# Kernel optimization log

Measured on AMD Instinct MI355X. Metric: run time of the kernel, lower is better.

## Reference

```python
import jax, jax.numpy as jnp
import numpy as np

B, IN_DIM, T = 4, 512, 4096
EMBED, HEADS, NB_FEAT = 1024, 16, 256
D_HEAD = EMBED // HEADS
EPS = 1e-6


def _orthogonal_random_matrix(key, nb_rows, nb_cols):
    # scaling==1 branch: sqrt(nb_cols) * Q from reduced QR of a Gaussian block
    block = jax.random.normal(key, (nb_rows, nb_cols), dtype=jnp.float32)
    q, _ = jnp.linalg.qr(block)
    return jnp.sqrt(jnp.float32(nb_cols)) * q


def setup_inputs() -> dict:
    key = jax.random.key(0)
    kx, kq, kk, kv, ko, kp = jax.random.split(key, 6)
    s = 1.0 / np.sqrt(IN_DIM)
    return {
        "x": jax.random.normal(kx, (B, IN_DIM, T), dtype=jnp.float32),
        "Wq": jax.random.normal(kq, (IN_DIM, EMBED), dtype=jnp.float32) * s,
        "Wk": jax.random.normal(kk, (IN_DIM, EMBED), dtype=jnp.float32) * s,
        "Wv": jax.random.normal(kv, (IN_DIM, EMBED), dtype=jnp.float32) * s,
        "Wo": jax.random.normal(ko, (EMBED, EMBED), dtype=jnp.float32) * (1.0 / np.sqrt(EMBED)),
        "proj": _orthogonal_random_matrix(kp, NB_FEAT, D_HEAD),
    }


def reference(x, Wq, Wk, Wv, Wo, proj):
    b, c, t = x.shape
    x_bt = jnp.transpose(x, (0, 2, 1))  # (B, T, in_dim)
    Q = (x_bt @ Wq).reshape(b, t, HEADS, D_HEAD)
    K = (x_bt @ Wk).reshape(b, t, HEADS, D_HEAD)
    V = (x_bt @ Wv).reshape(b, t, HEADS, D_HEAD)
    # exponential random-feature map
    Qp = jnp.exp(jnp.einsum('bthd,fd->bthf', Q, proj)) + EPS
    Kp = jnp.exp(jnp.einsum('bthd,fd->bthf', K, proj)) + EPS
    K_sum = Kp.sum(axis=1)                              # (B, H, F)
    KV = jnp.einsum('bthf,bthd->bhfd', Kp, V)           # (B, H, F, D)
    denom = jnp.maximum(jnp.einsum('bthf,bhf->bth', Qp, K_sum), 1e-6)
    numer = jnp.einsum('bthf,bhfd->bthd', Qp, KV)
    attn = numer / denom[..., None]                     # (B, T, H, D)
    out2 = attn.reshape(b, t, HEADS * D_HEAD) @ Wo      # (B, T, embed)
    cat = jnp.concatenate([x_bt, out2], axis=-1)        # (B, T, in_dim+embed)
    return jnp.transpose(cat, (0, 2, 1))
```

## Files before the change

kernel.cpp:

```cpp
#include <hip/hip_runtime.h>


constexpr int kB  = 4;
constexpr int kIn = 512;
constexpr int kT  = 4096;
constexpr int kE  = 1024;
constexpr int kH  = 16;
constexpr int kD  = 64;
constexpr int kF  = 256;
constexpr int kQKVs = 3072;

typedef __attribute__((ext_vector_type(8))) short bf16x8;
typedef __attribute__((ext_vector_type(4))) float f32x4;

__device__ __forceinline__ unsigned short f2bf(float f) {
    unsigned u = __float_as_uint(f);
    u += 0x7fff + ((u >> 16) & 1);
    return (unsigned short)(u >> 16);
}
__device__ __forceinline__ float bf2f(unsigned short s) {
    return __uint_as_float(((unsigned)s) << 16);
}
__device__ __forceinline__ void gload_lds16(const void* g, void* l) {
    __builtin_amdgcn_global_load_lds((const __attribute__((address_space(1))) void*)g,
                                     (__attribute__((address_space(3))) void*)l, 16, 0, 0);
}

__global__ __launch_bounds__(256) void zero_kernel(float* __restrict__ p, int n) {
    int i = blockIdx.x * 256 + threadIdx.x;
    if (i < n) p[i] = 0.f;
}

__global__ __launch_bounds__(256) void copy_x_kernel(const float* __restrict__ x,
                                                     float* __restrict__ out) {
    const int perB4 = kIn * kT / 4;
    int idx = blockIdx.x * 256 + threadIdx.x;
    if (idx < kB * perB4) {
        int b = idx / perB4, e = idx % perB4;
        ((float4*)out)[(size_t)b * ((kIn + kE) * kT / 4) + e] = ((const float4*)x)[idx];
    }
}

__global__ __launch_bounds__(256) void f2b_flat_kernel(const float* __restrict__ s,
                                                       unsigned short* __restrict__ d, int n4) {
    int i = blockIdx.x * 256 + threadIdx.x;
    if (i < n4) {
        float4 v = ((const float4*)s)[i];
        ushort4 o;
        o.x = f2bf(v.x); o.y = f2bf(v.y); o.z = f2bf(v.z); o.w = f2bf(v.w);
        ((ushort4*)d)[i] = o;
    }
}

__global__ __launch_bounds__(256) void trans_f2b_kernel(const float* __restrict__ src,
                                                        unsigned short* __restrict__ dst,
                                                        int R, int C,
                                                        long sstride, long dstride) {
    __shared__ float L[64][68];
    src += (size_t)blockIdx.z * sstride;
    dst += (size_t)blockIdx.z * dstride;
    const int c0 = blockIdx.x * 64, r0 = blockIdx.y * 64;
    const int tid = threadIdx.x;
#pragma unroll
    for (int it = 0; it < 4; ++it) {
        int lin = it * 256 + tid;
        int i = lin >> 4;
        int j4 = (lin & 15) * 4;
        float4 v = *(const float4*)(src + (size_t)(r0 + i) * C + c0 + j4);
        L[j4 + 0][i] = v.x; L[j4 + 1][i] = v.y; L[j4 + 2][i] = v.z; L[j4 + 3][i] = v.w;
    }
    __syncthreads();
#pragma unroll
    for (int it = 0; it < 4; ++it) {
        int lin = it * 256 + tid;
        int cc = lin >> 4;
        int r4 = (lin & 15) * 4;
        ushort4 o;
        o.x = f2bf(L[cc][r4 + 0]); o.y = f2bf(L[cc][r4 + 1]);
        o.z = f2bf(L[cc][r4 + 2]); o.w = f2bf(L[cc][r4 + 3]);
        *(ushort4*)(dst + (size_t)(c0 + cc) * R + r0 + r4) = o;
    }
}

__global__ __launch_bounds__(256) void trans_qkv_kernel(const float* __restrict__ Wq,
                                                        const float* __restrict__ Wk,
                                                        const float* __restrict__ Wv,
                                                        unsigned short* __restrict__ dst) {
    __shared__ float L[64][68];
    const int z = blockIdx.z;
    const float* src = (z == 0) ? Wq : (z == 1) ? Wk : Wv;
    dst += (size_t)z * kE * kIn;
    const int c0 = blockIdx.x * 64, r0 = blockIdx.y * 64;
    const int tid = threadIdx.x;
#pragma unroll
    for (int it = 0; it < 4; ++it) {
        int lin = it * 256 + tid;
        int i = lin >> 4;
        int j4 = (lin & 15) * 4;
        float4 v = *(const float4*)(src + (size_t)(r0 + i) * kE + c0 + j4);
        L[j4 + 0][i] = v.x; L[j4 + 1][i] = v.y; L[j4 + 2][i] = v.z; L[j4 + 3][i] = v.w;
    }
    __syncthreads();
#pragma unroll
    for (int it = 0; it < 4; ++it) {
        int lin = it * 256 + tid;
        int cc = lin >> 4;
        int r4 = (lin & 15) * 4;
        ushort4 o;
        o.x = f2bf(L[cc][r4 + 0]); o.y = f2bf(L[cc][r4 + 1]);
        o.z = f2bf(L[cc][r4 + 2]); o.w = f2bf(L[cc][r4 + 3]);
        *(ushort4*)(dst + (size_t)(c0 + cc) * kIn + r0 + r4) = o;
    }
}

__global__ __launch_bounds__(256) void gemm_mfma_b16(const unsigned short* __restrict__ A,
                                                     const unsigned short* __restrict__ Bt,
                                                     unsigned short* __restrict__ C,
                                                     int N, int K) {
    __shared__ unsigned short As[128 * 64];
    __shared__ unsigned short Bs[128 * 64];
    __shared__ float Tt[4][16 * 20];
    const int tid = threadIdx.x;
    const int lane = tid & 63, w = tid >> 6;
    const int col = lane & 15, quad = lane >> 4;
    const int n0 = blockIdx.x * 128, m0 = blockIdx.y * 128;
    const int wm = (w >> 1) * 64, wn = (w & 1) * 64;
    f32x4 acc[4][4];
#pragma unroll
    for (int i = 0; i < 4; ++i)
#pragma unroll
        for (int j = 0; j < 4; ++j) acc[i][j] = (f32x4){0.f, 0.f, 0.f, 0.f};

    const int swz = col & 7;
    for (int k0 = 0; k0 < K; k0 += 64) {
        __syncthreads();
#pragma unroll
        for (int i = 0; i < 4; ++i) {
            int p = (i * 4 + w) * 64 + lane;
            int row = p >> 3;
            int cg = ((p & 7) ^ (row & 7)) * 8;
            gload_lds16(A + (size_t)(m0 + row) * K + k0 + cg, &As[(i * 4 + w) * 512]);
            gload_lds16(Bt + (size_t)(n0 + row) * K + k0 + cg, &Bs[(i * 4 + w) * 512]);
        }
        __syncthreads();
#pragma unroll
        for (int s = 0; s < 2; ++s) {
            const int kc = ((s * 4 + quad) ^ swz) * 8;
            bf16x8 av[4], bv[4];
#pragma unroll
            for (int i = 0; i < 4; ++i)
                av[i] = *(const bf16x8*)&As[(wm + i * 16 + col) * 64 + kc];
#pragma unroll
            for (int j = 0; j < 4; ++j)
                bv[j] = *(const bf16x8*)&Bs[(wn + j * 16 + col) * 64 + kc];
#pragma unroll
            for (int i = 0; i < 4; ++i)
#pragma unroll
                for (int j = 0; j < 4; ++j)
                    acc[i][j] = __builtin_amdgcn_mfma_f32_16x16x32_bf16(av[i], bv[j], acc[i][j], 0, 0, 0);
        }
    }
    const int t2 = lane >> 2, n4 = (lane & 3) * 4;
#pragma unroll
    for (int i = 0; i < 4; ++i)
#pragma unroll
        for (int j = 0; j < 4; ++j) {
#pragma unroll
            for (int r = 0; r < 4; ++r)
                Tt[w][(quad * 4 + r) * 20 + col] = acc[i][j][r];
            float4 v = *(const float4*)&Tt[w][t2 * 20 + n4];
            ushort4 o;
            o.x = f2bf(v.x); o.y = f2bf(v.y); o.z = f2bf(v.z); o.w = f2bf(v.w);
            *(ushort4*)(C + (size_t)(m0 + wm + i * 16 + t2) * N + n0 + wn + j * 16 + n4) = o;
        }
}

__global__ __launch_bounds__(256) void gemm_mfma_out(const unsigned short* __restrict__ A,
                                                     const unsigned short* __restrict__ Bt,
                                                     float* __restrict__ out,
                                                     int N, int K) {
    __shared__ unsigned short As[128 * 64];
    __shared__ unsigned short Bs[128 * 64];
    __shared__ float Tt[4][16 * 20];
    const int tid = threadIdx.x;
    const int lane = tid & 63, w = tid >> 6;
    const int col = lane & 15, quad = lane >> 4;
    const int n0 = blockIdx.x * 128, m0 = blockIdx.y * 128;
    const int wm = (w >> 1) * 64, wn = (w & 1) * 64;
    f32x4 acc[4][4];
#pragma unroll
    for (int i = 0; i < 4; ++i)
#pragma unroll
        for (int j = 0; j < 4; ++j) acc[i][j] = (f32x4){0.f, 0.f, 0.f, 0.f};

    const int swz = col & 7;
    for (int k0 = 0; k0 < K; k0 += 64) {
        __syncthreads();
#pragma unroll
        for (int i = 0; i < 4; ++i) {
            int p = (i * 4 + w) * 64 + lane;
            int row = p >> 3;
            int cg = ((p & 7) ^ (row & 7)) * 8;
            gload_lds16(A + (size_t)(m0 + row) * K + k0 + cg, &As[(i * 4 + w) * 512]);
            gload_lds16(Bt + (size_t)(n0 + row) * K + k0 + cg, &Bs[(i * 4 + w) * 512]);
        }
        __syncthreads();
#pragma unroll
        for (int s = 0; s < 2; ++s) {
            const int kc = ((s * 4 + quad) ^ swz) * 8;
            bf16x8 av[4], bv[4];
#pragma unroll
            for (int i = 0; i < 4; ++i)
                av[i] = *(const bf16x8*)&As[(wm + i * 16 + col) * 64 + kc];
#pragma unroll
            for (int j = 0; j < 4; ++j)
                bv[j] = *(const bf16x8*)&Bs[(wn + j * 16 + col) * 64 + kc];
#pragma unroll
            for (int i = 0; i < 4; ++i)
#pragma unroll
                for (int j = 0; j < 4; ++j)
                    acc[i][j] = __builtin_amdgcn_mfma_f32_16x16x32_bf16(av[i], bv[j], acc[i][j], 0, 0, 0);
        }
    }
    const int b = m0 >> 12, t0 = m0 & 4095;
    float* dst = out + (size_t)b * (kIn + kE) * kT + (size_t)kIn * kT;
    const int n2 = lane >> 2, t4 = (lane & 3) * 4;
#pragma unroll
    for (int i = 0; i < 4; ++i)
#pragma unroll
        for (int j = 0; j < 4; ++j) {
            *(float4*)&Tt[w][col * 20 + quad * 4] =
                (float4){acc[i][j][0], acc[i][j][1], acc[i][j][2], acc[i][j][3]};
            float4 v = *(const float4*)&Tt[w][n2 * 20 + t4];
            *(float4*)(dst + (size_t)(n0 + wn + j * 16 + n2) * kT + t0 + wm + i * 16 + t4) = v;
        }
}

__global__ __launch_bounds__(256) void phaseA_mfma(const unsigned short* __restrict__ QKVb,
                                                   const unsigned short* __restrict__ projb,
                                                   float* __restrict__ KVg,
                                                   float* __restrict__ Ksumg) {
    __shared__ unsigned short Ks[64 * 64];
    __shared__ unsigned short VT[64 * 72];
    __shared__ unsigned short KpT[256 * 72];
    const int tid = threadIdx.x, lane = tid & 63, w = tid >> 6;
    const int col = lane & 15, quad = lane >> 4;
    const int bh = blockIdx.x, b = bh >> 4, h = bh & 15;
    const int grp = blockIdx.y;
    const int f0 = w * 64;
    const int swz = col & 7;

    bf16x8 bB[2][4];
#pragma unroll
    for (int s = 0; s < 2; ++s)
#pragma unroll
        for (int j = 0; j < 4; ++j)
            bB[s][j] = *(const bf16x8*)(projb + (size_t)(f0 + j * 16 + col) * 64 + s * 32 + quad * 8);

    f32x4 kvacc[4][4];
#pragma unroll
    for (int i = 0; i < 4; ++i)
#pragma unroll
        for (int j = 0; j < 4; ++j) kvacc[i][j] = (f32x4){0.f, 0.f, 0.f, 0.f};
    float ksum_acc[4] = {0.f, 0.f, 0.f, 0.f};

    for (int it = 0; it < 8; ++it) {
        const size_t rowbase = (size_t)(b * kT + grp * 512 + it * 64) * kQKVs + h * kD;
        __syncthreads();
#pragma unroll
        for (int i2 = 0; i2 < 2; ++i2) {
            int p = (i2 * 4 + w) * 64 + lane;
            int row = p >> 3;
            int cg = ((p & 7) ^ (row & 7)) * 8;
            gload_lds16(QKVb + rowbase + 1024 + (size_t)row * kQKVs + cg, &Ks[(i2 * 4 + w) * 512]);
        }
#pragma unroll
        for (int r = 0; r < 4; ++r) {
            int lin = r * 256 + tid;
            int t = lin >> 4, d4 = (lin & 15) * 4;
            ushort4 v = *(const ushort4*)(QKVb + rowbase + 2048 + (size_t)t * kQKVs + d4);
            VT[(d4 + 0) * 72 + t] = v.x; VT[(d4 + 1) * 72 + t] = v.y;
            VT[(d4 + 2) * 72 + t] = v.z; VT[(d4 + 3) * 72 + t] = v.w;
        }
        __syncthreads();
        bf16x8 av[2][4];
#pragma unroll
        for (int s = 0; s < 2; ++s)
#pragma unroll
            for (int i = 0; i < 4; ++i)
                av[s][i] = *(const bf16x8*)&Ks[(i * 16 + col) * 64 + ((s * 4 + quad) ^ swz) * 8];
#pragma unroll
        for (int j = 0; j < 4; ++j) {
            f32x4 sa[4];
#pragma unroll
            for (int i = 0; i < 4; ++i) sa[i] = (f32x4){0.f, 0.f, 0.f, 0.f};
#pragma unroll
            for (int s = 0; s < 2; ++s)
#pragma unroll
                for (int i = 0; i < 4; ++i)
                    sa[i] = __builtin_amdgcn_mfma_f32_16x16x32_bf16(av[s][i], bB[s][j], sa[i], 0, 0, 0);
            const int f = f0 + j * 16 + col;
#pragma unroll
            for (int i = 0; i < 4; ++i) {
                float e0 = __expf(sa[i][0]) + 1e-6f;
                float e1 = __expf(sa[i][1]) + 1e-6f;
                float e2 = __expf(sa[i][2]) + 1e-6f;
                float e3 = __expf(sa[i][3]) + 1e-6f;
                ksum_acc[j] += (e0 + e1) + (e2 + e3);
                ushort4 pk;
                pk.x = f2bf(e0); pk.y = f2bf(e1); pk.z = f2bf(e2); pk.w = f2bf(e3);
                *(ushort4*)&KpT[f * 72 + i * 16 + quad * 4] = pk;
            }
        }
#pragma unroll
        for (int s = 0; s < 2; ++s) {
            const int kc = s * 32 + quad * 8;
            bf16x8 a2[4], b2[4];
#pragma unroll
            for (int i = 0; i < 4; ++i)
                a2[i] = *(const bf16x8*)&KpT[(f0 + i * 16 + col) * 72 + kc];
#pragma unroll
            for (int jn = 0; jn < 4; ++jn)
                b2[jn] = *(const bf16x8*)&VT[(jn * 16 + col) * 72 + kc];
#pragma unroll
            for (int i = 0; i < 4; ++i)
#pragma unroll
                for (int jn = 0; jn < 4; ++jn)
                    kvacc[i][jn] = __builtin_amdgcn_mfma_f32_16x16x32_bf16(a2[i], b2[jn], kvacc[i][jn], 0, 0, 0);
        }
    }
    const size_t kvbase = (size_t)bh * (kF * kD);
#pragma unroll
    for (int i = 0; i < 4; ++i)
#pragma unroll
        for (int jn = 0; jn < 4; ++jn)
#pragma unroll
            for (int r = 0; r < 4; ++r)
                atomicAdd(&KVg[kvbase + (size_t)(f0 + i * 16 + quad * 4 + r) * kD + jn * 16 + col],
                          kvacc[i][jn][r]);
#pragma unroll
    for (int j = 0; j < 4; ++j) {
        float v = ksum_acc[j];
        v += __shfl_xor(v, 16);
        v += __shfl_xor(v, 32);
        if (quad == 0) atomicAdd(&Ksumg[(size_t)bh * kF + f0 + j * 16 + col], v);
    }
}

__global__ __launch_bounds__(256) void phaseB_mfma(const unsigned short* __restrict__ QKVb,
                                                   const unsigned short* __restrict__ projb,
                                                   const unsigned short* __restrict__ KVTb,
                                                   const float* __restrict__ Ksumg,
                                                   unsigned short* __restrict__ attnb) {
    __shared__ unsigned short Qs[64 * 64];
    __shared__ unsigned short Qp[64 * 264];
    __shared__ unsigned short KVTs[64 * 264];
    __shared__ float KsS[256];
    __shared__ float denp[4][64];
    const int tid = threadIdx.x, lane = tid & 63, w = tid >> 6;
    const int col = lane & 15, quad = lane >> 4;
    const int bh = blockIdx.x, b = bh >> 4, h = bh & 15;
    const int grp = blockIdx.y;
    const int f0 = w * 64;
    const int swz = col & 7;

    bf16x8 bB[2][4];
#pragma unroll
    for (int s = 0; s < 2; ++s)
#pragma unroll
        for (int j = 0; j < 4; ++j)
            bB[s][j] = *(const bf16x8*)(projb + (size_t)(f0 + j * 16 + col) * 64 + s * 32 + quad * 8);

#pragma unroll
    for (int r = 0; r < 8; ++r) {
        int lin = r * 256 + tid;
        int d = lin >> 5, fc8 = (lin & 31) * 8;
        *(bf16x8*)&KVTs[d * 264 + fc8] = *(const bf16x8*)(KVTb + (size_t)bh * 16384 + d * 256 + fc8);
    }
    KsS[tid] = Ksumg[(size_t)bh * kF + tid];

    for (int it = 0; it < 8; ++it) {
        const int tg0 = grp * 512 + it * 64;
        const size_t rowbase = (size_t)(b * kT + tg0) * kQKVs + h * kD;
        __syncthreads();
#pragma unroll
        for (int i2 = 0; i2 < 2; ++i2) {
            int p = (i2 * 4 + w) * 64 + lane;
            int row = p >> 3;
            int cg = ((p & 7) ^ (row & 7)) * 8;
            gload_lds16(QKVb + rowbase + (size_t)row * kQKVs + cg, &Qs[(i2 * 4 + w) * 512]);
        }
        __syncthreads();
        bf16x8 av[2][4];
#pragma unroll
        for (int s = 0; s < 2; ++s)
#pragma unroll
            for (int i = 0; i < 4; ++i)
                av[s][i] = *(const bf16x8*)&Qs[(i * 16 + col) * 64 + ((s * 4 + quad) ^ swz) * 8];
#pragma unroll
        for (int j = 0; j < 4; ++j) {
            f32x4 sa[4];
#pragma unroll
            for (int i = 0; i < 4; ++i) sa[i] = (f32x4){0.f, 0.f, 0.f, 0.f};
#pragma unroll
            for (int s = 0; s < 2; ++s)
#pragma unroll
                for (int i = 0; i < 4; ++i)
                    sa[i] = __builtin_amdgcn_mfma_f32_16x16x32_bf16(av[s][i], bB[s][j], sa[i], 0, 0, 0);
            const int f = f0 + j * 16 + col;
#pragma unroll
            for (int i = 0; i < 4; ++i) {
                const int tb = i * 16 + quad * 4;
                Qp[(tb + 0) * 264 + f] = f2bf(__expf(sa[i][0]) + 1e-6f);
                Qp[(tb + 1) * 264 + f] = f2bf(__expf(sa[i][1]) + 1e-6f);
                Qp[(tb + 2) * 264 + f] = f2bf(__expf(sa[i][2]) + 1e-6f);
                Qp[(tb + 3) * 264 + f] = f2bf(__expf(sa[i][3]) + 1e-6f);
            }
        }
        float dp = 0.f;
#pragma unroll
        for (int u = 0; u < 64; u += 8) {
            bf16x8 qv = *(const bf16x8*)&Qp[lane * 264 + f0 + u];
#pragma unroll
            for (int k2 = 0; k2 < 8; ++k2)
                dp += bf2f((unsigned short)qv[k2]) * KsS[f0 + u + k2];
        }
        denp[w][lane] = dp;
        __syncthreads();
        f32x4 nacc[4];
#pragma unroll
        for (int jn = 0; jn < 4; ++jn) nacc[jn] = (f32x4){0.f, 0.f, 0.f, 0.f};
#pragma unroll
        for (int s = 0; s < 8; ++s) {
            const int kc = s * 32 + quad * 8;
            bf16x8 aq = *(const bf16x8*)&Qp[(w * 16 + col) * 264 + kc];
#pragma unroll
            for (int jn = 0; jn < 4; ++jn) {
                bf16x8 bk = *(const bf16x8*)&KVTs[(jn * 16 + col) * 264 + kc];
                nacc[jn] = __builtin_amdgcn_mfma_f32_16x16x32_bf16(aq, bk, nacc[jn], 0, 0, 0);
            }
        }
#pragma unroll
        for (int r = 0; r < 4; ++r) {
            const int tl = w * 16 + quad * 4 + r;
            float den = denp[0][tl] + denp[1][tl] + denp[2][tl] + denp[3][tl];
            float rd = 1.f / fmaxf(den, 1e-6f);
            const size_t ob = (size_t)(b * kT + tg0 + tl) * kE + h * kD;
#pragma unroll
            for (int jn = 0; jn < 4; ++jn)
                attnb[ob + jn * 16 + col] = f2bf(nacc[jn][r] * rd);
        }
    }
}

extern "C" void kernel_launch(void* const* d_in, const int* in_sizes, int n_in,
                              void* d_out, int out_size, void* d_ws, size_t ws_size,
                              hipStream_t stream) {
    (void)in_sizes; (void)n_in; (void)out_size; (void)ws_size;
    const float* x    = (const float*)d_in[0];
    const float* Wq   = (const float*)d_in[1];
    const float* Wk   = (const float*)d_in[2];
    const float* Wv   = (const float*)d_in[3];
    const float* Wo   = (const float*)d_in[4];
    const float* proj = (const float*)d_in[5];
    float* out = (float*)d_out;

    char* ws = (char*)d_ws;
    unsigned short* QKVb  = (unsigned short*)(ws);
    unsigned short* attnb = (unsigned short*)(ws + 100663296);
    unsigned short* Abuf  = (unsigned short*)(ws + 100663296);
    unsigned short* Btqkv = (unsigned short*)(ws + 134217728);
    unsigned short* WoT   = (unsigned short*)(ws + 137363456);
    unsigned short* projb = (unsigned short*)(ws + 139460608);
    float*          KVg   = (float*)(ws + 139493376);
    float*          Ksumg = (float*)(ws + 143687680);
    unsigned short* KVTb  = (unsigned short*)(ws + 143753216);

    copy_x_kernel<<<dim3(8192), 256, 0, stream>>>(x, out);

    trans_f2b_kernel<<<dim3(64, 8, 4), 256, 0, stream>>>(x, Abuf, kIn, kT,
                                                         (long)kIn * kT, (long)kT * kIn);
    trans_qkv_kernel<<<dim3(16, 8, 3), 256, 0, stream>>>(Wq, Wk, Wv, Btqkv);
    trans_f2b_kernel<<<dim3(16, 16, 1), 256, 0, stream>>>(Wo, WoT, kE, kE, 0, 0);
    f2b_flat_kernel<<<dim3(16), 256, 0, stream>>>(proj, projb, kF * kD / 4);

    gemm_mfma_b16<<<dim3(24, 128), 256, 0, stream>>>(Abuf, Btqkv, QKVb, kQKVs, kIn);

    const int nz = kB * kH * kF * kD + kB * kH * kF;
    zero_kernel<<<dim3((nz + 255) / 256), 256, 0, stream>>>(KVg, nz);

    phaseA_mfma<<<dim3(64, 8), 256, 0, stream>>>(QKVb, projb, KVg, Ksumg);
    trans_f2b_kernel<<<dim3(1, 4, 64), 256, 0, stream>>>(KVg, KVTb, kF, kD,
                                                         (long)kF * kD, (long)kF * kD);
    phaseB_mfma<<<dim3(64, 8), 256, 0, stream>>>(QKVb, projb, KVTb, Ksumg, attnb);

    gemm_mfma_out<<<dim3(8, 128), 256, 0, stream>>>(attnb, WoT, out, kE, kE);
}
```

Baseline: 373.8 us.

## Replace 128x128 GEMMs with double-buffered 256x256 tile GEMMs with block swizzle

The QKV projection and output projection GEMMs move from 128x128 tiles with 4 waves to 256x256 tiles with 8 waves. The new main loop double-buffers LDS through 128KB of dynamic shared memory, so the next K-slice loads while the current one feeds MFMA, using manual vmcnt waits, barriers and setprio. Blocks are remapped with an 8-way grid swizzle to improve L2 locality. The larger tiles raise per-block data reuse, but give fewer blocks (256 for the output GEMM) and lower occupancy, which risks underfilling the CUs.

```diff
diff --git a/kernel.cpp b/kernel.cpp
--- a/kernel.cpp
+++ b/kernel.cpp
@@ -113,126 +113,163 @@
     }
 }
 
-__global__ __launch_bounds__(256) void gemm_mfma_b16(const unsigned short* __restrict__ A,
-                                                     const unsigned short* __restrict__ Bt,
-                                                     unsigned short* __restrict__ C,
-                                                     int N, int K) {
-    __shared__ unsigned short As[128 * 64];
-    __shared__ unsigned short Bs[128 * 64];
-    __shared__ float Tt[4][16 * 20];
-    const int tid = threadIdx.x;
-    const int lane = tid & 63, w = tid >> 6;
+__device__ __forceinline__ void stage256(const unsigned short* __restrict__ A,
+                                         const unsigned short* __restrict__ Bt,
+                                         int K, int m0, int n0, int kt,
+                                         unsigned short* AsB, unsigned short* BsB,
+                                         int tid) {
+    const int w = tid >> 6;
+    const size_t k0 = (size_t)kt * 64;
+#pragma unroll
+    for (int r = 0; r < 4; ++r) {
+        int idx = r * 512 + tid;
+        int row = idx >> 3;
+        int cg = (idx & 7) ^ (row & 7);
+        gload_lds16(A + (size_t)(m0 + row) * K + k0 + cg * 8, AsB + r * 4096 + w * 512);
+    }
+#pragma unroll
+    for (int r = 0; r < 4; ++r) {
+        int idx = r * 512 + tid;
+        int row = idx >> 3;
+        int cg = (idx & 7) ^ (row & 7);
+        gload_lds16(Bt + (size_t)(n0 + row) * K + k0 + cg * 8, BsB + r * 4096 + w * 512);
+    }
+}
+
+__device__ __forceinline__ void gemm256_mainloop(const unsigned short* __restrict__ A,
+                                                 const unsigned short* __restrict__ Bt,
+                                                 int K, int m0, int n0,
+                                                 unsigned short* smem,
+                                                 f32x4 (&acc)[8][4]) {
+    const int tid = threadIdx.x, lane = tid & 63, w = tid >> 6;
     const int col = lane & 15, quad = lane >> 4;
-    const int n0 = blockIdx.x * 128, m0 = blockIdx.y * 128;
-    const int wm = (w >> 1) * 64, wn = (w & 1) * 64;
-    f32x4 acc[4][4];
-#pragma unroll
-    for (int i = 0; i < 4; ++i)
+    const int wm = (w >> 2) * 128, wn = (w & 3) * 64;
+    const int swz = col & 7;
+    const int nt = K >> 6;
+    unsigned short* As0 = smem;
+    unsigned short* As1 = smem + 16384;
+    unsigned short* Bs0 = smem + 32768;
+    unsigned short* Bs1 = smem + 49152;
+
+    stage256(A, Bt, K, m0, n0, 0, As0, Bs0, tid);
+    stage256(A, Bt, K, m0, n0, 1, As1, Bs1, tid);
+#pragma unroll
+    for (int i = 0; i < 8; ++i)
 #pragma unroll
         for (int j = 0; j < 4; ++j) acc[i][j] = (f32x4){0.f, 0.f, 0.f, 0.f};
-
-    const int swz = col & 7;
-    for (int k0 = 0; k0 < K; k0 += 64) {
-        __syncthreads();
-#pragma unroll
-        for (int i = 0; i < 4; ++i) {
-            int p = (i * 4 + w) * 64 + lane;
-            int row = p >> 3;
-            int cg = ((p & 7) ^ (row & 7)) * 8;
-            gload_lds16(A + (size_t)(m0 + row) * K + k0 + cg, &As[(i * 4 + w) * 512]);
-            gload_lds16(Bt + (size_t)(n0 + row) * K + k0 + cg, &Bs[(i * 4 + w) * 512]);
-        }
-        __syncthreads();
-#pragma unroll
-        for (int s = 0; s < 2; ++s) {
-            const int kc = ((s * 4 + quad) ^ swz) * 8;
-            bf16x8 av[4], bv[4];
-#pragma unroll
-            for (int i = 0; i < 4; ++i)
-                av[i] = *(const bf16x8*)&As[(wm + i * 16 + col) * 64 + kc];
-#pragma unroll
-            for (int j = 0; j < 4; ++j)
-                bv[j] = *(const bf16x8*)&Bs[(wn + j * 16 + col) * 64 + kc];
-#pragma unroll
-            for (int i = 0; i < 4; ++i)
-#pragma unroll
-                for (int j = 0; j < 4; ++j)
-                    acc[i][j] = __builtin_amdgcn_mfma_f32_16x16x32_bf16(av[i], bv[j], acc[i][j], 0, 0, 0);
-        }
-    }
+    asm volatile("s_waitcnt vmcnt(8)" ::: "memory");
+    __builtin_amdgcn_s_barrier();
+    __builtin_amdgcn_sched_barrier(0);
+
+    for (int t = 0; ; ++t) {
+        const unsigned short* As_ = (t & 1) ? As1 : As0;
+        const unsigned short* Bs_ = (t & 1) ? Bs1 : Bs0;
+#pragma unroll
+        for (int q = 0; q < 4; ++q) {
+            const int ar0 = wm + (q >> 1) * 64;
+            const int bc0 = wn + (q & 1) * 32;
+            bf16x8 av[2][4], bv[2][2];
+#pragma unroll
+            for (int s = 0; s < 2; ++s) {
+                const int kc = ((s * 4 + quad) ^ swz) * 8;
+#pragma unroll
+                for (int i = 0; i < 4; ++i)
+                    av[s][i] = *(const bf16x8*)&As_[(ar0 + i * 16 + col) * 64 + kc];
+#pragma unroll
+                for (int j = 0; j < 2; ++j)
+                    bv[s][j] = *(const bf16x8*)&Bs_[(bc0 + j * 16 + col) * 64 + kc];
+            }
+            __builtin_amdgcn_s_setprio(1);
+#pragma unroll
+            for (int s = 0; s < 2; ++s)
+#pragma unroll
+                for (int i = 0; i < 4; ++i)
+#pragma unroll
+                    for (int j = 0; j < 2; ++j)
+                        acc[(q >> 1) * 4 + i][(q & 1) * 2 + j] =
+                            __builtin_amdgcn_mfma_f32_16x16x32_bf16(
+                                av[s][i], bv[s][j],
+                                acc[(q >> 1) * 4 + i][(q & 1) * 2 + j], 0, 0, 0);
+            __builtin_amdgcn_s_setprio(0);
+            __builtin_amdgcn_sched_barrier(0);
+            __builtin_amdgcn_s_barrier();
+            __builtin_amdgcn_sched_barrier(0);
+        }
+        if (t == nt - 1) break;
+        if (t + 2 < nt) {
+            stage256(A, Bt, K, m0, n0, t + 2, (t & 1) ? As1 : As0, (t & 1) ? Bs1 : Bs0, tid);
+            asm volatile("s_waitcnt vmcnt(8)" ::: "memory");
+        } else {
+            asm volatile("s_waitcnt vmcnt(0)" ::: "memory");
+        }
+        __builtin_amdgcn_sched_barrier(0);
+        __builtin_amdgcn_s_barrier();
+        __builtin_amdgcn_sched_barrier(0);
+    }
+}
+
+__global__ __launch_bounds__(512) void gemm256_b16(const unsigned short* __restrict__ A,
+                                                   const unsigned short* __restrict__ Bt,
+                                                   unsigned short* __restrict__ C,
+                                                   int N, int K, int ntN) {
+    extern __shared__ unsigned short smem_us[];
+    const int tid = threadIdx.x, lane = tid & 63, w = tid >> 6;
+    const int col = lane & 15, quad = lane >> 4;
+    const int wm = (w >> 2) * 128, wn = (w & 3) * 64;
+    const int bid = blockIdx.x;
+    const int qch = gridDim.x >> 3;
+    const int swb = (bid & 7) * qch + (bid >> 3);
+    const int mt = swb / ntN, ntl = swb - mt * ntN;
+    const int m0 = mt * 256, n0 = ntl * 256;
+
+    f32x4 acc[8][4];
+    gemm256_mainloop(A, Bt, K, m0, n0, smem_us, acc);
+
+    float* Tw = (float*)smem_us + w * 336;
     const int t2 = lane >> 2, n4 = (lane & 3) * 4;
 #pragma unroll
-    for (int i = 0; i < 4; ++i)
-#pragma unroll
-        for (int j = 0; j < 4; ++j) {
+    for (int ri = 0; ri < 8; ++ri)
+#pragma unroll
+        for (int cj = 0; cj < 4; ++cj) {
 #pragma unroll
             for (int r = 0; r < 4; ++r)
-                Tt[w][(quad * 4 + r) * 20 + col] = acc[i][j][r];
-            float4 v = *(const float4*)&Tt[w][t2 * 20 + n4];
+                Tw[(quad * 4 + r) * 20 + col] = acc[ri][cj][r];
+            float4 v = *(const float4*)&Tw[t2 * 20 + n4];
             ushort4 o;
             o.x = f2bf(v.x); o.y = f2bf(v.y); o.z = f2bf(v.z); o.w = f2bf(v.w);
-            *(ushort4*)(C + (size_t)(m0 + wm + i * 16 + t2) * N + n0 + wn + j * 16 + n4) = o;
-        }
-}
-
-__global__ __launch_bounds__(256) void gemm_mfma_out(const unsigned short* __restrict__ A,
-                                                     const unsigned short* __restrict__ Bt,
-                                                     float* __restrict__ out,
-                                                     int N, int K) {
-    __shared__ unsigned short As[128 * 64];
-    __shared__ unsigned short Bs[128 * 64];
-    __shared__ float Tt[4][16 * 20];
-    const int tid = threadIdx.x;
-    const int lane = tid & 63, w = tid >> 6;
+            *(ushort4*)(C + (size_t)(m0 + wm + ri * 16 + t2) * N + n0 + wn + cj * 16 + n4) = o;
+        }
+}
+
+__global__ __launch_bounds__(512) void gemm256_out(const unsigned short* __restrict__ A,
+                                                   const unsigned short* __restrict__ Bt,
+                                                   float* __restrict__ out,
+                                                   int N, int K, int ntN) {
+    extern __shared__ unsigned short smem_us[];
+    const int tid = threadIdx.x, lane = tid & 63, w = tid >> 6;
     const int col = lane & 15, quad = lane >> 4;
-    const int n0 = blockIdx.x * 128, m0 = blockIdx.y * 128;
-    const int wm = (w >> 1) * 64, wn = (w & 1) * 64;
-    f32x4 acc[4][4];
-#pragma unroll
-    for (int i = 0; i < 4; ++i)
-#pragma unroll
-        for (int j = 0; j < 4; ++j) acc[i][j] = (f32x4){0.f, 0.f, 0.f, 0.f};
-
-    const int swz = col & 7;
-    for (int k0 = 0; k0 < K; k0 += 64) {
-        __syncthreads();
-#pragma unroll
-        for (int i = 0; i < 4; ++i) {
-            int p = (i * 4 + w) * 64 + lane;
-            int row = p >> 3;
-            int cg = ((p & 7) ^ (row & 7)) * 8;
-            gload_lds16(A + (size_t)(m0 + row) * K + k0 + cg, &As[(i * 4 + w) * 512]);
-            gload_lds16(Bt + (size_t)(n0 + row) * K + k0 + cg, &Bs[(i * 4 + w) * 512]);
-        }
-        __syncthreads();
-#pragma unroll
-        for (int s = 0; s < 2; ++s) {
-            const int kc = ((s * 4 + quad) ^ swz) * 8;
-            bf16x8 av[4], bv[4];
-#pragma unroll
-            for (int i = 0; i < 4; ++i)
-                av[i] = *(const bf16x8*)&As[(wm + i * 16 + col) * 64 + kc];
-#pragma unroll
-            for (int j = 0; j < 4; ++j)
-                bv[j] = *(const bf16x8*)&Bs[(wn + j * 16 + col) * 64 + kc];
-#pragma unroll
-            for (int i = 0; i < 4; ++i)
-#pragma unroll
-                for (int j = 0; j < 4; ++j)
-                    acc[i][j] = __builtin_amdgcn_mfma_f32_16x16x32_bf16(av[i], bv[j], acc[i][j], 0, 0, 0);
-        }
-    }
+    const int wm = (w >> 2) * 128, wn = (w & 3) * 64;
+    const int bid = blockIdx.x;
+    const int qch = gridDim.x >> 3;
+    const int swb = (bid & 7) * qch + (bid >> 3);
+    const int mt = swb / ntN, ntl = swb - mt * ntN;
+    const int m0 = mt * 256, n0 = ntl * 256;
+
+    f32x4 acc[8][4];
+    gemm256_mainloop(A, Bt, K, m0, n0, smem_us, acc);
+
     const int b = m0 >> 12, t0 = m0 & 4095;
     float* dst = out + (size_t)b * (kIn + kE) * kT + (size_t)kIn * kT;
+    float* Tw = (float*)smem_us + w * 336;
     const int n2 = lane >> 2, t4 = (lane & 3) * 4;
 #pragma unroll
-    for (int i = 0; i < 4; ++i)
-#pragma unroll
-        for (int j = 0; j < 4; ++j) {
-            *(float4*)&Tt[w][col * 20 + quad * 4] =
-                (float4){acc[i][j][0], acc[i][j][1], acc[i][j][2], acc[i][j][3]};
-            float4 v = *(const float4*)&Tt[w][n2 * 20 + t4];
-            *(float4*)(dst + (size_t)(n0 + wn + j * 16 + n2) * kT + t0 + wm + i * 16 + t4) = v;
+    for (int ri = 0; ri < 8; ++ri)
+#pragma unroll
+        for (int cj = 0; cj < 4; ++cj) {
+            *(float4*)&Tw[col * 20 + quad * 4] =
+                (float4){acc[ri][cj][0], acc[ri][cj][1], acc[ri][cj][2], acc[ri][cj][3]};
+            float4 v = *(const float4*)&Tw[n2 * 20 + t4];
+            *(float4*)(dst + (size_t)(n0 + wn + cj * 16 + n2) * kT + t0 + wm + ri * 16 + t4) = v;
         }
 }
 
@@ -465,6 +502,15 @@
     const float* proj = (const float*)d_in[5];
     float* out = (float*)d_out;
 
+    static int attr_done = 0;
+    if (!attr_done) {
+        hipFuncSetAttribute((const void*)gemm256_b16,
+                            hipFuncAttributeMaxDynamicSharedMemorySize, 131072);
+        hipFuncSetAttribute((const void*)gemm256_out,
+                            hipFuncAttributeMaxDynamicSharedMemorySize, 131072);
+        attr_done = 1;
+    }
+
     char* ws = (char*)d_ws;
     unsigned short* QKVb  = (unsigned short*)(ws);
     unsigned short* attnb = (unsigned short*)(ws + 100663296);
@@ -484,7 +530,7 @@
     trans_f2b_kernel<<<dim3(16, 16, 1), 256, 0, stream>>>(Wo, WoT, kE, kE, 0, 0);
     f2b_flat_kernel<<<dim3(16), 256, 0, stream>>>(proj, projb, kF * kD / 4);
 
-    gemm_mfma_b16<<<dim3(24, 128), 256, 0, stream>>>(Abuf, Btqkv, QKVb, kQKVs, kIn);
+    gemm256_b16<<<dim3(768), 512, 131072, stream>>>(Abuf, Btqkv, QKVb, kQKVs, kIn, 12);
 
     const int nz = kB * kH * kF * kD + kB * kH * kF;
     zero_kernel<<<dim3((nz + 255) / 256), 256, 0, stream>>>(KVg, nz);
@@ -494,5 +540,5 @@
                                                          (long)kF * kD, (long)kF * kD);
     phaseB_mfma<<<dim3(64, 8), 256, 0, stream>>>(QKVb, projb, KVTb, Ksumg, attnb);
 
-    gemm_mfma_out<<<dim3(8, 128), 256, 0, stream>>>(attnb, WoT, out, kE, kE);
-}
+    gemm256_out<<<dim3(256), 512, 131072, stream>>>(attnb, WoT, out, kE, kE, 4);
+}
```

Result: no change. 371.8 us (-0.5%).
